# Kernel optimization log

Hardware: AMD Instinct MI355X
Metric: run time of the kernel (lower is better)

The kernel has to match this reference:

```python
import jax, jax.numpy as jnp
import numpy as np

N_FILTERS = 1024
N_HEADS = 16


def setup_inputs() -> dict:
    key = jax.random.key(0)
    k1, k2, k3 = jax.random.split(key, 3)
    x = jax.random.normal(k1, (8, 1024, N_FILTERS), dtype=jnp.float32)
    # VarianceScaling(0.02) ~ small dense init; 0.02*sqrt(1/fan_in) scale approximated
    w_qkv = jax.random.normal(k2, (N_FILTERS, N_FILTERS * 3), dtype=jnp.float32) * (0.02 / N_FILTERS) ** 0.5
    w_out = jax.random.normal(k3, (N_FILTERS, N_FILTERS), dtype=jnp.float32) * (0.02 / N_FILTERS) ** 0.5
    return {"x": x, "w_qkv": w_qkv, "w_out": w_out}


def reference(x, w_qkv, w_out):
    b, n, c = x.shape
    h = N_HEADS
    d = c // h
    qkv = jnp.einsum('bnc,ce->bne', x, w_qkv)  # [b, n, 3c]
    q, k, v = jnp.split(qkv, 3, axis=-1)
    # b n (h d) -> b h n d
    to_heads = lambda t: t.reshape(b, n, h, d).transpose(0, 2, 1, 3)
    q, k, v = to_heads(q), to_heads(k), to_heads(v)
    scale = jnp.sqrt(jnp.asarray(c, jnp.float32))  # NOTE: sqrt(n_filters), matches source
    attn = jnp.einsum('bhnd,bhmd->bhnm', q, k) / scale
    attn = jax.nn.softmax(attn, axis=-1)
    out = jnp.einsum('bhnm,bhmd->bhnd', attn, v)
    out = out.transpose(0, 2, 1, 3).reshape(b, n, c)  # b h n d -> b n (h d)
    return jnp.einsum('bnc,co->bno', out, w_out)
```

## Files before the change

### kernel.cpp

```cpp
#include <hip/hip_runtime.h>
#include <hip/hip_bf16.h>

typedef __bf16 bf16_t;
typedef __bf16 bf16x8 __attribute__((ext_vector_type(8)));
typedef __bf16 bf16x4 __attribute__((ext_vector_type(4)));
typedef float f32x4 __attribute__((ext_vector_type(4)));

constexpr int LD = 3072;

#define MFMA_16x16x32(a, b, c) __builtin_amdgcn_mfma_f32_16x16x32_bf16((a), (b), (c), 0, 0, 0)

#define GLOAD_LDS16(g, l)                                               \
  __builtin_amdgcn_global_load_lds(                                     \
      (const __attribute__((address_space(1))) void*)(g),               \
      (__attribute__((address_space(3))) void*)(l), 16, 0, 0)

#define TRREAD(dst, addr, imm) \
  asm volatile("ds_read_b64_tr_b16 %0, %1 offset:" imm : "=v"(dst) : "v"(addr))

#define BAR __builtin_amdgcn_s_barrier()
#define LGKM0 do { asm volatile("s_waitcnt lgkmcnt(0)" ::: "memory"); \
                   __builtin_amdgcn_sched_barrier(0); } while (0)

__global__ void cvt_kernel(const float* __restrict__ in, bf16_t* __restrict__ out, int n8) {
  int i = blockIdx.x * blockDim.x + threadIdx.x;
  if (i >= n8) return;
  const float4 a = reinterpret_cast<const float4*>(in)[2 * i];
  const float4 c = reinterpret_cast<const float4*>(in)[2 * i + 1];
  bf16x8 o;
  o[0] = (bf16_t)a.x; o[1] = (bf16_t)a.y; o[2] = (bf16_t)a.z; o[3] = (bf16_t)a.w;
  o[4] = (bf16_t)c.x; o[5] = (bf16_t)c.y; o[6] = (bf16_t)c.z; o[7] = (bf16_t)c.w;
  reinterpret_cast<bf16x8*>(out)[i] = o;
}

__global__ void tcvt_kernel(const float* __restrict__ in, bf16_t* __restrict__ out, int R, int C) {
  __shared__ float tile[32][33];
  const int c0 = blockIdx.x * 32, r0 = blockIdx.y * 32;
  const int tx = threadIdx.x & 31, ty = threadIdx.x >> 5;
#pragma unroll
  for (int i = 0; i < 32; i += 8)
    tile[ty + i][tx] = in[(size_t)(r0 + ty + i) * C + (c0 + tx)];
  __syncthreads();
#pragma unroll
  for (int i = 0; i < 32; i += 8)
    out[(size_t)(c0 + ty + i) * R + (r0 + tx)] = (bf16_t)tile[tx][ty + i];
}

__global__ __launch_bounds__(512, 2) void gemm_qkv_256(
    const bf16_t* __restrict__ A, const bf16_t* __restrict__ Bt,
    bf16_t* __restrict__ C, float q_scale) {
  constexpr int K = 1024;
  extern __shared__ char smem[];
  char* asB = smem;
  char* bsB = smem + 65536;

  const int t = threadIdx.x;
  const int lane = t & 63, wave = t >> 6;
  const int l15 = lane & 15, lg = lane >> 4;
  const int wr = wave >> 2, wc = wave & 3;

  const int bid = blockIdx.x;
  const int wg = (bid & 7) * 48 + (bid >> 3);
  const int brow = (wg & 31) * 256;
  const int bcol = (wg >> 5) * 256;

  const int srow = t >> 3;
  const int schk = (t & 7) ^ (srow & 7);
  const bf16_t* aS = A + (size_t)(brow + srow) * K + schk * 8;
  const bf16_t* bS = Bt + (size_t)(bcol + srow) * K + schk * 8;
  const int ldst = t * 8;

#define STG_A(T, H) do {                                                      \
    const bf16_t* _s = aS + (size_t)((H) * 128) * K + (T) * 64;               \
    bf16_t* _d = (bf16_t*)(asB + ((T) & 1) * 32768 + (H) * 16384) + ldst;     \
    GLOAD_LDS16(_s, _d);                                                      \
    GLOAD_LDS16(_s + (size_t)64 * K, _d + 4096);                              \
  } while (0)
#define STG_B(T, H) do {                                                      \
    const bf16_t* _s = bS + (size_t)((H) * 128) * K + (T) * 64;               \
    bf16_t* _d = (bf16_t*)(bsB + ((T) & 1) * 32768 + (H) * 16384) + ldst;     \
    GLOAD_LDS16(_s, _d);                                                      \
    GLOAD_LDS16(_s + (size_t)64 * K, _d + 4096);                              \
  } while (0)

  const int rx = l15 & 7;
  const unsigned c0 = ((unsigned)(lg ^ rx)) << 4;
  const unsigned c1 = ((unsigned)((4 | lg) ^ rx)) << 4;
  const unsigned a_rd = (unsigned)(wr * 16384 + l15 * 128);
  const unsigned b_rd = (unsigned)((wc >> 1) * 16384 + (wc & 1) * 8192 + l15 * 128);

  f32x4 acc[8][4] = {};
  bf16x8 af[4][2], bfr[2][2];

#define RD_AF(BUF, MH) do { _Pragma("unroll")                                 \
    for (int m = 0; m < 4; ++m) {                                             \
      const char* _p = asB + (BUF) * 32768 + a_rd + ((MH) * 4 + m) * 2048;    \
      af[m][0] = *(const bf16x8*)(_p + c0);                                   \
      af[m][1] = *(const bf16x8*)(_p + c1); } } while (0)
#define RD_BF(BUF, NH) do { _Pragma("unroll")                                 \
    for (int n = 0; n < 2; ++n) {                                             \
      const char* _p = bsB + (BUF) * 32768 + b_rd + ((NH) * 2 + n) * 2048;    \
      bfr[n][0] = *(const bf16x8*)(_p + c0);                                  \
      bfr[n][1] = *(const bf16x8*)(_p + c1); } } while (0)
#define MM16(MH, NH) do {                                                     \
    __builtin_amdgcn_s_setprio(1);                                            \
    _Pragma("unroll")                                                         \
    for (int m = 0; m < 4; ++m) { _Pragma("unroll")                           \
      for (int n = 0; n < 2; ++n) {                                           \
        acc[(MH)*4+m][(NH)*2+n] =                                             \
            MFMA_16x16x32(af[m][0], bfr[n][0], acc[(MH)*4+m][(NH)*2+n]);      \
        acc[(MH)*4+m][(NH)*2+n] =                                             \
            MFMA_16x16x32(af[m][1], bfr[n][1], acc[(MH)*4+m][(NH)*2+n]); } }  \
    __builtin_amdgcn_s_setprio(0); } while (0)

  STG_A(0, 0); STG_A(0, 1); STG_B(0, 0); STG_B(0, 1); STG_A(1, 0);
  asm volatile("s_waitcnt vmcnt(2)" ::: "memory");
  BAR;

  for (int i = 0; i < 8; ++i) {
    const int T1 = 2 * i + 1, T2 = 2 * i + 2, T3 = 2 * i + 3;
    const bool pf = (i < 7);
    STG_A(T1, 1);
    RD_AF(0, 0); RD_BF(0, 0);
    BAR; LGKM0; MM16(0, 0); BAR;
    STG_B(T1, 0);
    RD_BF(0, 1);
    BAR; LGKM0; MM16(0, 1); BAR;
    STG_B(T1, 1);
    RD_AF(0, 1);
    BAR; LGKM0; MM16(1, 1); BAR;
    if (pf) STG_A(T2, 0);
    RD_BF(0, 0);
    BAR; LGKM0; MM16(1, 0);
    if (pf) asm volatile("s_waitcnt vmcnt(2)" ::: "memory");
    else    asm volatile("s_waitcnt vmcnt(0)" ::: "memory");
    BAR;
    if (pf) STG_A(T2, 1);
    RD_AF(1, 0); RD_BF(1, 0);
    BAR; LGKM0; MM16(0, 0); BAR;
    if (pf) STG_B(T2, 0);
    RD_BF(1, 1);
    BAR; LGKM0; MM16(0, 1); BAR;
    if (pf) STG_B(T2, 1);
    RD_AF(1, 1);
    BAR; LGKM0; MM16(1, 1); BAR;
    if (pf) STG_A(T3, 0);
    RD_BF(1, 0);
    BAR; LGKM0; MM16(1, 0);
    asm volatile("s_waitcnt vmcnt(2)" ::: "memory");
    BAR;
  }

  const float sc = (bcol < 1024) ? q_scale : 1.0f;
  const int crow0 = brow + wr * 128 + lg * 4;
  const int ccol0 = bcol + wc * 64 + l15;
#pragma unroll
  for (int m = 0; m < 8; ++m)
#pragma unroll
    for (int n = 0; n < 4; ++n)
#pragma unroll
      for (int r = 0; r < 4; ++r)
        C[(size_t)(crow0 + m * 16 + r) * 3072 + ccol0 + n * 16] =
            (bf16_t)(acc[m][n][r] * sc);
#undef STG_A
#undef STG_B
#undef RD_AF
#undef RD_BF
#undef MM16
}

template <typename OutT>
__global__ __launch_bounds__(512, 1) void gemm_bt_128x256(
    const bf16_t* __restrict__ A, const bf16_t* __restrict__ Bt,
    OutT* __restrict__ C, int N, int nrowblk, int q_cols, float q_scale) {
  constexpr int K = 1024;
  extern __shared__ char smem[];
  char* asB = smem;
  char* bsB = smem + 49152;

  const int t = threadIdx.x;
  const int lane = t & 63, wave = t >> 6;
  const int l15 = lane & 15, lg = lane >> 4;
  const int wr = wave >> 2, wc = wave & 3;

  const int cpx = (int)gridDim.x >> 3;
  const int bid = blockIdx.x;
  const int wg = (bid & 7) * cpx + (bid >> 3);
  const int brow = (wg % nrowblk) * 128;
  const int bcol = (wg / nrowblk) * 256;

  const int srow = t >> 3;
  const int schk = (t & 7) ^ (srow & 7);
  const bf16_t* aS = A + (size_t)(brow + srow) * K + schk * 8;
  const bf16_t* bS = Bt + (size_t)(bcol + srow) * K + schk * 8;
  const int ldst = t * 8;

#define STG_A(T, BUF) do {                                               \
    const bf16_t* _s = aS + (T) * 64;                                    \
    bf16_t* _d = (bf16_t*)(asB + (BUF) * 16384) + ldst;                  \
    GLOAD_LDS16(_s, _d);                                                 \
    GLOAD_LDS16(_s + (size_t)64 * K, _d + 4096);                         \
  } while (0)
#define STG_B(T, H, BUF) do {                                            \
    const bf16_t* _s = bS + (size_t)((H) * 128) * K + (T) * 64;          \
    bf16_t* _d = (bf16_t*)(bsB + (BUF) * 32768 + (H) * 16384) + ldst;    \
    GLOAD_LDS16(_s, _d);                                                 \
    GLOAD_LDS16(_s + (size_t)64 * K, _d + 4096);                         \
  } while (0)

  const int rx = l15 & 7;
  const unsigned c0 = ((unsigned)(lg ^ rx)) << 4;
  const unsigned c1 = ((unsigned)((4 | lg) ^ rx)) << 4;
  const unsigned a_rd = (unsigned)(wr * 8192 + l15 * 128);
  const unsigned b_rd = (unsigned)((wc >> 1) * 16384 + (wc & 1) * 8192 + l15 * 128);

  f32x4 acc[4][4] = {};
  bf16x8 af[2][2], bfr[4][2];

#define RD_AF(BUF, MH) do { _Pragma("unroll")                            \
    for (int m = 0; m < 2; ++m) {                                        \
      const char* _p = asB + (BUF) * 16384 + a_rd + ((MH) * 2 + m) * 2048; \
      af[m][0] = *(const bf16x8*)(_p + c0);                              \
      af[m][1] = *(const bf16x8*)(_p + c1); } } while (0)
#define RD_BF(BUF) do { _Pragma("unroll")                                \
    for (int n = 0; n < 4; ++n) {                                        \
      const char* _p = bsB + (BUF) * 32768 + b_rd + n * 2048;            \
      bfr[n][0] = *(const bf16x8*)(_p + c0);                             \
      bfr[n][1] = *(const bf16x8*)(_p + c1); } } while (0)
#define MM(MH) do {                                                      \
    __builtin_amdgcn_s_setprio(1);                                       \
    _Pragma("unroll")                                                    \
    for (int m = 0; m < 2; ++m) { _Pragma("unroll")                      \
      for (int n = 0; n < 4; ++n) {                                      \
        acc[(MH)*2+m][n] =                                               \
            MFMA_16x16x32(af[m][0], bfr[n][0], acc[(MH)*2+m][n]);        \
        acc[(MH)*2+m][n] =                                               \
            MFMA_16x16x32(af[m][1], bfr[n][1], acc[(MH)*2+m][n]); } }    \
    __builtin_amdgcn_s_setprio(0); } while (0)

  STG_A(0, 0); STG_B(0, 0, 0); STG_B(0, 1, 0);
  STG_A(1, 1); STG_B(1, 0, 1); STG_B(1, 1, 1);
  asm volatile("s_waitcnt vmcnt(6)" ::: "memory");
  BAR;

  int bc = 0;
  for (int T = 0; T < 16; ++T) {
    const bool pf = (T + 2 < 16);
    const int bs = (bc >= 1) ? (bc - 1) : 2;
    if (pf) { STG_A(T + 2, bs); STG_B(T + 2, 0, bs); }
    RD_AF(bc, 0);
    RD_BF(bc);
    BAR; LGKM0; MM(0); BAR;
    if (pf) STG_B(T + 2, 1, bs);
    RD_AF(bc, 1);
    BAR; LGKM0; MM(1);
    if (pf) asm volatile("s_waitcnt vmcnt(6)" ::: "memory");
    else    asm volatile("s_waitcnt vmcnt(0)" ::: "memory");
    BAR;
    bc = (bc == 2) ? 0 : bc + 1;
  }

  const float sc = (bcol < q_cols) ? q_scale : 1.0f;
  const int crow0 = brow + wr * 64 + lg * 4;
  const int ccol0 = bcol + wc * 64 + l15;
#pragma unroll
  for (int m = 0; m < 4; ++m)
#pragma unroll
    for (int n = 0; n < 4; ++n)
#pragma unroll
      for (int r = 0; r < 4; ++r)
        C[(size_t)(crow0 + m * 16 + r) * N + ccol0 + n * 16] =
            (OutT)(acc[m][n][r] * sc);
#undef STG_A
#undef STG_B
#undef RD_AF
#undef RD_BF
#undef MM
}

__device__ __forceinline__ unsigned pack_bf16_pair(float a, float b) {
  union { __hip_bfloat162 h; unsigned u; } c;
  c.h = __float22bfloat162_rn(float2{a, b});
  return c.u;
}

__global__ __launch_bounds__(256, 3) void attn_kernel(const bf16_t* __restrict__ qkv,
                                                      bf16_t* __restrict__ ctx) {
  __shared__ bf16_t Ks[2][4096];
  __shared__ bf16_t Vs[2][4096];
  const int tid = threadIdx.x, lane = tid & 63, wave = tid >> 6;
  const int l15 = lane & 15, lg = (lane >> 4) & 3;
  const int flat = blockIdx.x;
  const int xcd = flat & 7, rr = flat >> 3;
  const int qt = rr & 7;
  const int hb = xcd * 16 + (rr >> 3);
  const int h = hb & 15, b = hb >> 4;
  const size_t base = (size_t)b * 1024 * LD;
  const int qbase = qt * 128 + wave * 32;

  bf16x8 qa[2][2];
#pragma unroll
  for (int s = 0; s < 2; s++) {
    const bf16_t* qp = qkv + base + (size_t)(qbase + s * 16 + l15) * LD + h * 64 + lg * 8;
    qa[s][0] = *reinterpret_cast<const bf16x8*>(qp);
    qa[s][1] = *reinterpret_cast<const bf16x8*>(qp + 32);
  }

  const bf16_t* Kb = qkv + base + 1024 + h * 64;
  const bf16_t* Vb = qkv + base + 2048 + h * 64;

  const int krr = lane >> 3;
  const int kcc = (lane & 7) ^ krr;
  const bf16_t* ksrc0 = Kb + (size_t)(wave * 16 + krr) * LD + kcc * 8;
  const bf16_t* ksrc1 = ksrc0 + (size_t)8 * LD;

  const int vd0 = (lane & 1) * 8 + wave * 16;
  const int vkv = ((lane >> 1) & 3) + ((lane >> 3) & 3) * 4 + (lane >> 5) * 16;
  const bf16_t* vsrc0 = Vb + (size_t)vkv * LD + vd0;
  const bf16_t* vsrc1 = vsrc0 + (size_t)32 * LD;

  bf16_t* ksb = &Ks[0][0];
  bf16_t* vsb = &Vs[0][0];
  const char* ksr = (const char*)&Ks[0][0];
  const unsigned vs_byte =
      (unsigned)(size_t)(__attribute__((address_space(3))) void*)(&Vs[0][0]);
  const unsigned tr_lane = vs_byte + lane * 8;

  const int rx7 = l15 & 7;
  const unsigned kb0 = (unsigned)(l15 * 128 + ((lg ^ rx7) << 4));
  const unsigned kb1 = (unsigned)(l15 * 128 + (((4 | lg) ^ rx7) << 4));

  bf16x8 ones;
#pragma unroll
  for (int j = 0; j < 8; j++) ones[j] = (bf16_t)1.0f;

  f32x4 dn[2] = {};
  f32x4 oacc[2][4] = {};

  GLOAD_LDS16(ksrc0, ksb + wave * 1024);
  GLOAD_LDS16(ksrc1, ksb + wave * 1024 + 512);
  GLOAD_LDS16(vsrc0, vsb + wave * 1024);
  GLOAD_LDS16(vsrc1, vsb + wave * 1024 + 512);
  ksrc0 += (size_t)64 * LD; ksrc1 += (size_t)64 * LD;
  vsrc0 += (size_t)64 * LD; vsrc1 += (size_t)64 * LD;
  __syncthreads();

  for (int t = 0; t < 16; t++) {
    const int cur = t & 1;
    if (t < 15) {
      bf16_t* kd = ksb + (cur ^ 1) * 4096 + wave * 1024;
      bf16_t* vd = vsb + (cur ^ 1) * 4096 + wave * 1024;
      GLOAD_LDS16(ksrc0, kd);
      GLOAD_LDS16(ksrc1, kd + 512);
      GLOAD_LDS16(vsrc0, vd);
      GLOAD_LDS16(vsrc1, vd + 512);
      ksrc0 += (size_t)64 * LD; ksrc1 += (size_t)64 * LD;
      vsrc0 += (size_t)64 * LD; vsrc1 += (size_t)64 * LD;
    }

    f32x4 sacc[2][4] = {};
    const char* kt = ksr + cur * 8192;
    __builtin_amdgcn_s_setprio(1);
#pragma unroll
    for (int tt = 0; tt < 4; tt++) {
      const bf16x8 k0 = *reinterpret_cast<const bf16x8*>(kt + tt * 2048 + kb0);
      const bf16x8 k1 = *reinterpret_cast<const bf16x8*>(kt + tt * 2048 + kb1);
      sacc[0][tt] = MFMA_16x16x32(k0, qa[0][0], sacc[0][tt]);
      sacc[0][tt] = MFMA_16x16x32(k1, qa[0][1], sacc[0][tt]);
      sacc[1][tt] = MFMA_16x16x32(k0, qa[1][0], sacc[1][tt]);
      sacc[1][tt] = MFMA_16x16x32(k1, qa[1][1], sacc[1][tt]);
    }
    __builtin_amdgcn_s_setprio(0);

    const unsigned ta = tr_lane + (unsigned)cur * 8192;
    bf16x4 tl0, th0, tl2, th2, tl4, th4, tl6, th6;
    TRREAD(tl0, ta, "0");    TRREAD(th0, ta, "512");
    TRREAD(tl2, ta, "2048"); TRREAD(th2, ta, "2560");
    TRREAD(tl4, ta, "4096"); TRREAD(th4, ta, "4608");
    TRREAD(tl6, ta, "6144"); TRREAD(th6, ta, "6656");
    __builtin_amdgcn_sched_barrier(0);

    unsigned pu[16];
#pragma unroll
    for (int tt = 0; tt < 4; tt++) {
      const float a0 = __builtin_exp2f(sacc[0][tt][0]);
      const float a1 = __builtin_exp2f(sacc[0][tt][1]);
      const float a2 = __builtin_exp2f(sacc[0][tt][2]);
      const float a3 = __builtin_exp2f(sacc[0][tt][3]);
      pu[(tt >> 1) * 4 + (tt & 1) * 2 + 0] = pack_bf16_pair(a0, a1);
      pu[(tt >> 1) * 4 + (tt & 1) * 2 + 1] = pack_bf16_pair(a2, a3);
      const float b0 = __builtin_exp2f(sacc[1][tt][0]);
      const float b1 = __builtin_exp2f(sacc[1][tt][1]);
      const float b2 = __builtin_exp2f(sacc[1][tt][2]);
      const float b3 = __builtin_exp2f(sacc[1][tt][3]);
      pu[8 + (tt >> 1) * 4 + (tt & 1) * 2 + 0] = pack_bf16_pair(b0, b1);
      pu[8 + (tt >> 1) * 4 + (tt & 1) * 2 + 1] = pack_bf16_pair(b2, b3);
    }
    bf16x8 pa[2][2];
    pa[0][0] = *reinterpret_cast<bf16x8*>(&pu[0]);
    pa[0][1] = *reinterpret_cast<bf16x8*>(&pu[4]);
    pa[1][0] = *reinterpret_cast<bf16x8*>(&pu[8]);
    pa[1][1] = *reinterpret_cast<bf16x8*>(&pu[12]);

    dn[0] = MFMA_16x16x32(pa[0][0], ones, dn[0]);
    dn[0] = MFMA_16x16x32(pa[0][1], ones, dn[0]);
    dn[1] = MFMA_16x16x32(pa[1][0], ones, dn[1]);
    dn[1] = MFMA_16x16x32(pa[1][1], ones, dn[1]);

    bf16x4 tl1, th1, tl3, th3, tl5, th5, tl7, th7;
    TRREAD(tl1, ta, "1024"); TRREAD(th1, ta, "1536");
    TRREAD(tl3, ta, "3072"); TRREAD(th3, ta, "3584");
    TRREAD(tl5, ta, "5120"); TRREAD(th5, ta, "5632");
    TRREAD(tl7, ta, "7168"); TRREAD(th7, ta, "7680");

    asm volatile("s_waitcnt lgkmcnt(8)" ::: "memory");
    __builtin_amdgcn_sched_barrier(0);
    {
      bf16x8 vb0[4];
      vb0[0] = __builtin_shufflevector(tl0, th0, 0, 1, 2, 3, 4, 5, 6, 7);
      vb0[1] = __builtin_shufflevector(tl2, th2, 0, 1, 2, 3, 4, 5, 6, 7);
      vb0[2] = __builtin_shufflevector(tl4, th4, 0, 1, 2, 3, 4, 5, 6, 7);
      vb0[3] = __builtin_shufflevector(tl6, th6, 0, 1, 2, 3, 4, 5, 6, 7);
      __builtin_amdgcn_s_setprio(1);
#pragma unroll
      for (int s = 0; s < 2; s++)
#pragma unroll
        for (int dt = 0; dt < 4; dt++)
          oacc[s][dt] = MFMA_16x16x32(pa[s][0], vb0[dt], oacc[s][dt]);
      __builtin_amdgcn_s_setprio(0);
    }

    asm volatile("s_waitcnt lgkmcnt(0)" ::: "memory");
    __builtin_amdgcn_sched_barrier(0);
    {
      bf16x8 vb1[4];
      vb1[0] = __builtin_shufflevector(tl1, th1, 0, 1, 2, 3, 4, 5, 6, 7);
      vb1[1] = __builtin_shufflevector(tl3, th3, 0, 1, 2, 3, 4, 5, 6, 7);
      vb1[2] = __builtin_shufflevector(tl5, th5, 0, 1, 2, 3, 4, 5, 6, 7);
      vb1[3] = __builtin_shufflevector(tl7, th7, 0, 1, 2, 3, 4, 5, 6, 7);
      __builtin_amdgcn_s_setprio(1);
#pragma unroll
      for (int s = 0; s < 2; s++)
#pragma unroll
        for (int dt = 0; dt < 4; dt++)
          oacc[s][dt] = MFMA_16x16x32(pa[s][1], vb1[dt], oacc[s][dt]);
      __builtin_amdgcn_s_setprio(0);
    }

    __syncthreads();
  }

#pragma unroll
  for (int s = 0; s < 2; s++) {
#pragma unroll
    for (int r = 0; r < 4; r++) {
      const float inv = 1.0f / dn[s][r];
      const size_t row = (size_t)(b * 1024 + qbase + s * 16 + lg * 4 + r);
#pragma unroll
      for (int dt = 0; dt < 4; dt++)
        ctx[row * 1024 + h * 64 + dt * 16 + l15] = (bf16_t)(oacc[s][dt][r] * inv);
    }
  }
}

extern "C" void kernel_launch(void* const* d_in, const int* in_sizes, int n_in,
                              void* d_out, int out_size, void* d_ws, size_t ws_size,
                              hipStream_t stream) {
  (void)in_sizes; (void)n_in; (void)out_size; (void)ws_size;
  const float* x = (const float*)d_in[0];
  const float* w_qkv = (const float*)d_in[1];
  const float* w_out = (const float*)d_in[2];
  float* out = (float*)d_out;
  char* ws = (char*)d_ws;

  bf16_t* x_b   = (bf16_t*)(ws);
  bf16_t* qkv_b = (bf16_t*)(ws + (size_t)(16 << 20));
  bf16_t* wqT   = (bf16_t*)(ws + (size_t)(64 << 20));
  bf16_t* woT   = (bf16_t*)(ws + (size_t)(70 << 20));
  bf16_t* ctx_b = (bf16_t*)(ws + (size_t)(72 << 20));

  const float qsc = 0.045084220027780106f;

  cvt_kernel<<<8388608 / 8 / 256, 256, 0, stream>>>(x, x_b, 8388608 / 8);
  tcvt_kernel<<<dim3(3072 / 32, 1024 / 32), 256, 0, stream>>>(w_qkv, wqT, 1024, 3072);
  tcvt_kernel<<<dim3(1024 / 32, 1024 / 32), 256, 0, stream>>>(w_out, woT, 1024, 1024);

  gemm_qkv_256<<<384, 512, 131072, stream>>>(x_b, wqT, qkv_b, qsc);
  attn_kernel<<<1024, 256, 0, stream>>>(qkv_b, ctx_b);
  gemm_bt_128x256<float><<<256, 512, 147456, stream>>>(
      ctx_b, woT, out, 1024, 64, 0, 1.0f);
}
```

Before: 161.6 us.

## Merge conversion kernels into one launch and triple-buffer attention K/V loads

The three fp32-to-bf16 conversion/transpose kernels become a single prep kernel that dispatches on block index, removing two launches. The attention kernel moves from double to triple buffering of K/V tiles in LDS: it prefetches two tiles ahead and waits with vmcnt(4) before a plain barrier instead of __syncthreads. This is meant to hide more global-load latency, at the cost of extra LDS per block (48KB), which may limit occupancy.

```diff
diff --git a/kernel.cpp b/kernel.cpp
--- a/kernel.cpp
+++ b/kernel.cpp
@@ -22,20 +22,27 @@
 #define LGKM0 do { asm volatile("s_waitcnt lgkmcnt(0)" ::: "memory"); \
                    __builtin_amdgcn_sched_barrier(0); } while (0)
 
-__global__ void cvt_kernel(const float* __restrict__ in, bf16_t* __restrict__ out, int n8) {
-  int i = blockIdx.x * blockDim.x + threadIdx.x;
-  if (i >= n8) return;
-  const float4 a = reinterpret_cast<const float4*>(in)[2 * i];
-  const float4 c = reinterpret_cast<const float4*>(in)[2 * i + 1];
-  bf16x8 o;
-  o[0] = (bf16_t)a.x; o[1] = (bf16_t)a.y; o[2] = (bf16_t)a.z; o[3] = (bf16_t)a.w;
-  o[4] = (bf16_t)c.x; o[5] = (bf16_t)c.y; o[6] = (bf16_t)c.z; o[7] = (bf16_t)c.w;
-  reinterpret_cast<bf16x8*>(out)[i] = o;
-}
-
-__global__ void tcvt_kernel(const float* __restrict__ in, bf16_t* __restrict__ out, int R, int C) {
+__global__ __launch_bounds__(256) void prep_kernel(
+    const float* __restrict__ x, bf16_t* __restrict__ x_b,
+    const float* __restrict__ w_qkv, bf16_t* __restrict__ wqT,
+    const float* __restrict__ w_out, bf16_t* __restrict__ woT) {
+  const int blk = blockIdx.x;
+  if (blk < 4096) {
+    const int i = blk * 256 + threadIdx.x;
+    const float4 a = reinterpret_cast<const float4*>(x)[2 * i];
+    const float4 c = reinterpret_cast<const float4*>(x)[2 * i + 1];
+    bf16x8 o;
+    o[0] = (bf16_t)a.x; o[1] = (bf16_t)a.y; o[2] = (bf16_t)a.z; o[3] = (bf16_t)a.w;
+    o[4] = (bf16_t)c.x; o[5] = (bf16_t)c.y; o[6] = (bf16_t)c.z; o[7] = (bf16_t)c.w;
+    reinterpret_cast<bf16x8*>(x_b)[i] = o;
+    return;
+  }
   __shared__ float tile[32][33];
-  const int c0 = blockIdx.x * 32, r0 = blockIdx.y * 32;
+  const float* in; bf16_t* outp; int C, bx, by;
+  if (blk < 7168) { const int i = blk - 4096; in = w_qkv; outp = wqT; C = 3072; bx = i % 96; by = i / 96; }
+  else            { const int i = blk - 7168; in = w_out; outp = woT; C = 1024; bx = i & 31; by = i >> 5; }
+  constexpr int R = 1024;
+  const int c0 = bx * 32, r0 = by * 32;
   const int tx = threadIdx.x & 31, ty = threadIdx.x >> 5;
 #pragma unroll
   for (int i = 0; i < 32; i += 8)
@@ -43,7 +50,7 @@
   __syncthreads();
 #pragma unroll
   for (int i = 0; i < 32; i += 8)
-    out[(size_t)(c0 + ty + i) * R + (r0 + tx)] = (bf16_t)tile[tx][ty + i];
+    outp[(size_t)(c0 + ty + i) * R + (r0 + tx)] = (bf16_t)tile[tx][ty + i];
 }
 
 __global__ __launch_bounds__(512, 2) void gemm_qkv_256(
@@ -286,8 +293,8 @@
 
 __global__ __launch_bounds__(256, 3) void attn_kernel(const bf16_t* __restrict__ qkv,
                                                       bf16_t* __restrict__ ctx) {
-  __shared__ bf16_t Ks[2][4096];
-  __shared__ bf16_t Vs[2][4096];
+  __shared__ bf16_t Ks[3][4096];
+  __shared__ bf16_t Vs[3][4096];
   const int tid = threadIdx.x, lane = tid & 63, wave = tid >> 6;
   const int l15 = lane & 15, lg = (lane >> 4) & 3;
   const int flat = blockIdx.x;
@@ -337,29 +344,29 @@
   f32x4 dn[2] = {};
   f32x4 oacc[2][4] = {};
 
-  GLOAD_LDS16(ksrc0, ksb + wave * 1024);
-  GLOAD_LDS16(ksrc1, ksb + wave * 1024 + 512);
-  GLOAD_LDS16(vsrc0, vsb + wave * 1024);
-  GLOAD_LDS16(vsrc1, vsb + wave * 1024 + 512);
-  ksrc0 += (size_t)64 * LD; ksrc1 += (size_t)64 * LD;
-  vsrc0 += (size_t)64 * LD; vsrc1 += (size_t)64 * LD;
-  __syncthreads();
-
+#define STAGE(BUF, T) do {                                               \
+    const size_t _go = (size_t)(T) * 64 * LD;                            \
+    bf16_t* _kd = ksb + (BUF) * 4096 + wave * 1024;                      \
+    bf16_t* _vd = vsb + (BUF) * 4096 + wave * 1024;                      \
+    GLOAD_LDS16(ksrc0 + _go, _kd);                                       \
+    GLOAD_LDS16(ksrc1 + _go, _kd + 512);                                 \
+    GLOAD_LDS16(vsrc0 + _go, _vd);                                       \
+    GLOAD_LDS16(vsrc1 + _go, _vd + 512);                                 \
+  } while (0)
+
+  STAGE(0, 0);
+  STAGE(1, 1);
+  asm volatile("s_waitcnt vmcnt(4)" ::: "memory");
+  __builtin_amdgcn_sched_barrier(0);
+  BAR;
+
+  int bc = 0;
   for (int t = 0; t < 16; t++) {
-    const int cur = t & 1;
-    if (t < 15) {
-      bf16_t* kd = ksb + (cur ^ 1) * 4096 + wave * 1024;
-      bf16_t* vd = vsb + (cur ^ 1) * 4096 + wave * 1024;
-      GLOAD_LDS16(ksrc0, kd);
-      GLOAD_LDS16(ksrc1, kd + 512);
-      GLOAD_LDS16(vsrc0, vd);
-      GLOAD_LDS16(vsrc1, vd + 512);
-      ksrc0 += (size_t)64 * LD; ksrc1 += (size_t)64 * LD;
-      vsrc0 += (size_t)64 * LD; vsrc1 += (size_t)64 * LD;
-    }
+    const int bsg = (bc == 0) ? 2 : bc - 1;
+    if (t < 14) STAGE(bsg, t + 2);
 
     f32x4 sacc[2][4] = {};
-    const char* kt = ksr + cur * 8192;
+    const char* kt = ksr + bc * 8192;
     __builtin_amdgcn_s_setprio(1);
 #pragma unroll
     for (int tt = 0; tt < 4; tt++) {
@@ -372,7 +379,7 @@
     }
     __builtin_amdgcn_s_setprio(0);
 
-    const unsigned ta = tr_lane + (unsigned)cur * 8192;
+    const unsigned ta = tr_lane + (unsigned)(bc * 8192);
     bf16x4 tl0, th0, tl2, th2, tl4, th4, tl6, th6;
     TRREAD(tl0, ta, "0");    TRREAD(th0, ta, "512");
     TRREAD(tl2, ta, "2048"); TRREAD(th2, ta, "2560");
@@ -447,7 +454,12 @@
       __builtin_amdgcn_s_setprio(0);
     }
 
-    __syncthreads();
+    if (t < 14) asm volatile("s_waitcnt vmcnt(4)" ::: "memory");
+    else        asm volatile("s_waitcnt vmcnt(0)" ::: "memory");
+    __builtin_amdgcn_sched_barrier(0);
+    BAR;
+
+    bc = (bc == 2) ? 0 : bc + 1;
   }
 
 #pragma unroll
@@ -461,6 +473,7 @@
         ctx[row * 1024 + h * 64 + dt * 16 + l15] = (bf16_t)(oacc[s][dt][r] * inv);
     }
   }
+#undef STAGE
 }
 
 extern "C" void kernel_launch(void* const* d_in, const int* in_sizes, int n_in,
@@ -481,10 +494,7 @@
 
   const float qsc = 0.045084220027780106f;
 
-  cvt_kernel<<<8388608 / 8 / 256, 256, 0, stream>>>(x, x_b, 8388608 / 8);
-  tcvt_kernel<<<dim3(3072 / 32, 1024 / 32), 256, 0, stream>>>(w_qkv, wqT, 1024, 3072);
-  tcvt_kernel<<<dim3(1024 / 32, 1024 / 32), 256, 0, stream>>>(w_out, woT, 1024, 1024);
-
+  prep_kernel<<<8192, 256, 0, stream>>>(x, x_b, w_qkv, wqT, w_out, woT);
   gemm_qkv_256<<<384, 512, 131072, stream>>>(x_b, wqT, qkv_b, qsc);
   attn_kernel<<<1024, 256, 0, stream>>>(qkv_b, ctx_b);
   gemm_bt_128x256<float><<<256, 512, 147456, stream>>>(
```

Measured after the change: 161.1 us. About the same (-0.3%).
